# Optimization experiments

Measured on AMD Instinct MI355X. Metric: run time of the kernel, lower is better.

Reference implementation:

```python
import jax, jax.numpy as jnp
import numpy as np

NS, L, H = 8, 2048, 1024
M, E, K = 4096, 8, 2
EPS = 1e-9

def setup_inputs() -> dict:
    key = jax.random.key(0)
    ks = jax.random.split(key, 5)
    s = 0.02
    return {
        "x": jax.random.normal(ks[0], (NS, L, H), jnp.float32),
        "Wr": jax.random.normal(ks[1], (H, E), jnp.float32) * s,
        "br": jnp.zeros((E,), jnp.float32),
        "W1": jax.random.normal(ks[2], (E, H, M), jnp.float32) * s,
        "b1": jnp.zeros((E, M), jnp.float32),
        "W2": jax.random.normal(ks[3], (E, M, H), jnp.float32) * s,
        "b2": jnp.zeros((E, H), jnp.float32),
    }

def reference(x, Wr, br, W1, b1, W2, b2):
    ns, seq, h = x.shape
    flat = x.reshape(-1, h)                      # (N, H); grouping only reshapes, math is per-token
    logits = flat @ Wr + br                      # (N, E)
    probs = jax.nn.softmax(logits, axis=-1)
    vals, idx = jax.lax.top_k(probs, K)          # (N, K)
    w = vals / (jnp.sum(vals, axis=-1, keepdims=True) + EPS)
    out_acc = jnp.zeros_like(flat)
    weight_acc = jnp.zeros((flat.shape[0],), flat.dtype)
    for e in range(E):                           # fixed small expert loop
        we = jnp.sum(w * (idx == e), axis=-1)    # (N,) combine weight for expert e
        hmid = jax.nn.gelu(flat @ W1[e] + b1[e], approximate=False)
        y = hmid @ W2[e] + b2[e]
        out_acc = out_acc + we[:, None] * y
        weight_acc = weight_acc + we
    out = out_acc / (weight_acc[:, None] + EPS)
    return out.reshape(ns, seq, h)
```

## Files before the change

kernel.cpp:

```cpp
#include <hip/hip_runtime.h>
#include <hip/hip_bf16.h>
#include <math.h>

#define NTOK 16384
#define HDIM 1024
#define MDIM 4096
#define NEXP 8
#define EPSV 1e-9f
#define RTOK 32

typedef unsigned short u16;
typedef __attribute__((ext_vector_type(4))) float f32x4;
typedef __attribute__((ext_vector_type(8))) __bf16 bf16x8;
typedef __attribute__((ext_vector_type(8))) unsigned short u16x8;
typedef __attribute__((ext_vector_type(4))) unsigned short u16x4;

#define ASYNC_COPY16(gptr, lptr) \
    __builtin_amdgcn_global_load_lds( \
        (const __attribute__((address_space(1))) void*)(gptr), \
        (__attribute__((address_space(3))) void*)(lptr), 16, 0, 0)

static __device__ __forceinline__ u16 f2bf(float f) {
    unsigned int u = __builtin_bit_cast(unsigned int, f);
    u += 0x7fff + ((u >> 16) & 1);
    return (u16)(u >> 16);
}

static __device__ __forceinline__ float gelu_f(float v) {
    float z2 = -1.5957691216f * v * (1.f + 0.044715f * v * v);
    return v / (1.f + __expf(z2));
}

__global__ __launch_bounds__(256) void router_kernel(
    const float* __restrict__ x, const float* __restrict__ Wr,
    const float* __restrict__ br,
    int* __restrict__ counts, int* __restrict__ ltok, float* __restrict__ lcf,
    u16* __restrict__ xb)
{
    __shared__ int   lcount[NEXP];
    __shared__ int   lbase[NEXP];
    __shared__ int   ltokL[NEXP][RTOK];
    __shared__ float lcfL[NEXP][RTOK];

    int t = threadIdx.x;
    if (t < NEXP) lcount[t] = 0;
    __syncthreads();

    int wave = t >> 6, lane = t & 63;

    for (int it = 0; it < RTOK / 4; ++it) {
        int tok = blockIdx.x * RTOK + it * 4 + wave;
        const float* xr = x + (size_t)tok * HDIM + lane * 16;

        f32x4 xv[4];
        #pragma unroll
        for (int q = 0; q < 4; q++) xv[q] = *reinterpret_cast<const f32x4*>(xr + q * 4);

        u16x8 ob0, ob1;
        #pragma unroll
        for (int j = 0; j < 4; j++) {
            ob0[j]     = f2bf(xv[0][j]);
            ob0[4 + j] = f2bf(xv[1][j]);
            ob1[j]     = f2bf(xv[2][j]);
            ob1[4 + j] = f2bf(xv[3][j]);
        }
        u16* xo = xb + (size_t)tok * HDIM + lane * 16;
        *reinterpret_cast<u16x8*>(xo)     = ob0;
        *reinterpret_cast<u16x8*>(xo + 8) = ob1;

        f32x4 acc0 = {0.f, 0.f, 0.f, 0.f};
        f32x4 acc1 = {0.f, 0.f, 0.f, 0.f};
        #pragma unroll
        for (int q = 0; q < 4; q++) {
            #pragma unroll
            for (int j = 0; j < 4; j++) {
                int h = lane * 16 + q * 4 + j;
                const float* wrow = Wr + (size_t)h * NEXP;
                f32x4 w0 = *reinterpret_cast<const f32x4*>(wrow);
                f32x4 w1 = *reinterpret_cast<const f32x4*>(wrow + 4);
                acc0 += xv[q][j] * w0;
                acc1 += xv[q][j] * w1;
            }
        }
        float a[NEXP];
        #pragma unroll
        for (int e = 0; e < 4; e++) { a[e] = acc0[e]; a[4 + e] = acc1[e]; }
        #pragma unroll
        for (int e = 0; e < NEXP; e++) {
            #pragma unroll
            for (int s = 1; s < 64; s <<= 1) a[e] += __shfl_xor(a[e], s, 64);
        }
        if (lane == 0) {
            float l[NEXP], m = -1e30f;
            #pragma unroll
            for (int e = 0; e < NEXP; e++) { l[e] = a[e] + br[e]; m = fmaxf(m, l[e]); }
            float p[NEXP], s = 0.f;
            #pragma unroll
            for (int e = 0; e < NEXP; e++) { p[e] = expf(l[e] - m); s += p[e]; }
            int i0 = 0; float v0 = p[0];
            #pragma unroll
            for (int e = 1; e < NEXP; e++) if (p[e] > v0) { v0 = p[e]; i0 = e; }
            int i1 = -1; float v1 = -1.f;
            #pragma unroll
            for (int e = 0; e < NEXP; e++) if (e != i0 && p[e] > v1) { v1 = p[e]; i1 = e; }
            v0 /= s; v1 /= s;
            float sw = v0 + v1;
            float w0 = v0 / (sw + EPSV), w1 = v1 / (sw + EPSV);
            float wa = w0 + w1;
            float c0 = w0 / (wa + EPSV), c1 = w1 / (wa + EPSV);
            int q0 = atomicAdd(&lcount[i0], 1);
            ltokL[i0][q0] = tok; lcfL[i0][q0] = c0;
            int q1 = atomicAdd(&lcount[i1], 1);
            ltokL[i1][q1] = tok; lcfL[i1][q1] = c1;
        }
    }
    __syncthreads();
    if (t < NEXP) lbase[t] = atomicAdd(&counts[t], lcount[t]);
    __syncthreads();
    #pragma unroll
    for (int e = 0; e < NEXP; e++) {
        int n = lcount[e], b = lbase[e];
        for (int j = t; j < n; j += 256) {
            ltok[e * NTOK + b + j] = ltokL[e][j];
            lcf[e * NTOK + b + j]  = lcfL[e][j];
        }
    }
}

__global__ void bases_kernel(const int* __restrict__ counts, int* __restrict__ bases)
{
    if (threadIdx.x == 0) {
        int acc = 0;
        #pragma unroll
        for (int e = 0; e < NEXP; e++) { bases[e] = acc; acc += counts[e]; }
    }
}

__global__ __launch_bounds__(256) void transpose_cvt_kernel(
    const float* __restrict__ in, u16* __restrict__ out, int R, int C)
{
    __shared__ float tile[32][33];
    const float* ine = in + (size_t)blockIdx.z * R * C;
    u16* oute = out + (size_t)blockIdx.z * R * C;
    int r0 = blockIdx.y * 32, c0 = blockIdx.x * 32;
    int t = threadIdx.x;
    int r = t >> 3, cq = t & 7;
    f32x4 v = *reinterpret_cast<const f32x4*>(ine + (size_t)(r0 + r) * C + c0 + cq * 4);
    #pragma unroll
    for (int j = 0; j < 4; j++) tile[r][cq * 4 + j] = v[j];
    __syncthreads();
    int c = t >> 3, rq = t & 7;
    u16x4 o;
    #pragma unroll
    for (int j = 0; j < 4; j++) o[j] = f2bf(tile[rq * 4 + j][c]);
    *reinterpret_cast<u16x4*>(oute + (size_t)(c0 + c) * R + r0 + rq * 4) = o;
}

template<int EPI, int GX, int GY>
__global__ __launch_bounds__(256) void gemm_kernel(
    const u16* __restrict__ A,
    const u16* __restrict__ BT_all,
    const float* __restrict__ bias_all,
    const int* __restrict__ counts,
    const int* __restrict__ bases,
    const int* __restrict__ ltok,
    const float* __restrict__ lcf,
    u16* __restrict__ hmid,
    float* __restrict__ out,
    int K, int P, int Astride, int eStart)
{
    int gz = gridDim.z;
    int nwg = GX * GY * gz;
    int orig = blockIdx.x + GX * (blockIdx.y + GY * blockIdx.z);
    int q = nwg >> 3, r = nwg & 7;
    int xcd = orig & 7, sub = orig >> 3;
    int wgid = (xcd < r ? xcd * (q + 1) : r * (q + 1) + (xcd - r) * q) + sub;
    int bx = wgid & (GX - 1);
    int rem = wgid / GX;
    int by = rem & (GY - 1);
    int bz = rem / GY;

    int e = eStart + bz;
    int nrows = counts[e];
    int row0 = by * 128;
    if (row0 >= nrows) return;
    int p0 = bx * 128;
    int slotbase = bases[e];
    const u16*   BT   = BT_all + (size_t)e * P * K;
    const float* bias = bias_all + (size_t)e * P;
    const int*   lte  = ltok + (size_t)e * NTOK;
    const float* lcfe = lcf  + (size_t)e * NTOK;

    __shared__ u16 As[2][128][64];
    __shared__ u16 Bs[2][128][64];

    int t = threadIdx.x;
    int wv = t >> 6, lane = t & 63;
    int lrow8 = lane >> 3;
    int lcol8 = lane & 7;
    int schunk = lcol8 ^ lrow8;

    const u16* aptr[4];
    const u16* bptr[4];
    #pragma unroll
    for (int i = 0; i < 4; i++) {
        int pos  = row0 + wv * 32 + i * 8 + lrow8;
        int posc = min(pos, nrows - 1);
        int arow = (EPI == 0) ? lte[posc] : (slotbase + posc);
        aptr[i] = A + (size_t)arow * Astride + schunk * 8;
        int prow = p0 + wv * 32 + i * 8 + lrow8;
        bptr[i] = BT + (size_t)prow * K + schunk * 8;
    }

    int wr = (wv >> 1) * 64, wc = (wv & 1) * 64;
    int lr = lane & 15, lg = lane >> 4;
    int lr7 = lr & 7;

    f32x4 acc[4][4];
    #pragma unroll
    for (int m = 0; m < 4; m++)
        #pragma unroll
        for (int nn = 0; nn < 4; nn++) acc[m][nn] = (f32x4){0.f, 0.f, 0.f, 0.f};

    auto stage = [&](int buf, int k0) {
        #pragma unroll
        for (int i = 0; i < 4; i++) {
            ASYNC_COPY16(aptr[i] + k0, &As[buf][wv * 32 + i * 8][0]);
            ASYNC_COPY16(bptr[i] + k0, &Bs[buf][wv * 32 + i * 8][0]);
        }
    };

    stage(0, 0);
    __syncthreads();
    int nk = K >> 6;
    int cur = 0;
    for (int ks = 0; ks < nk; ks++) {
        if (ks + 1 < nk) stage(cur ^ 1, (ks + 1) << 6);
        #pragma unroll
        for (int kk = 0; kk < 64; kk += 32) {
            bf16x8 af[4], bfr[4];
            #pragma unroll
            for (int m = 0; m < 4; m++)
                af[m] = *reinterpret_cast<const bf16x8*>(
                    &As[cur][wr + m * 16 + lr][((((kk >> 3) + lg) ^ lr7)) * 8]);
            #pragma unroll
            for (int nn = 0; nn < 4; nn++)
                bfr[nn] = *reinterpret_cast<const bf16x8*>(
                    &Bs[cur][wc + nn * 16 + lr][((((kk >> 3) + lg) ^ lr7)) * 8]);
            #pragma unroll
            for (int m = 0; m < 4; m++)
                #pragma unroll
                for (int nn = 0; nn < 4; nn++)
                    acc[m][nn] = __builtin_amdgcn_mfma_f32_16x16x32_bf16(
                        af[m], bfr[nn], acc[m][nn], 0, 0, 0);
        }
        __syncthreads();
        cur ^= 1;
    }

    if (EPI == 0) {
        #pragma unroll
        for (int m = 0; m < 4; m++) {
            #pragma unroll
            for (int r2 = 0; r2 < 4; r2++) {
                int pos = row0 + wr + m * 16 + lg * 4 + r2;
                if (pos < nrows) {
                    size_t ho = (size_t)(slotbase + pos) * MDIM;
                    #pragma unroll
                    for (int nn = 0; nn < 4; nn++) {
                        int col = p0 + wc + nn * 16 + lr;
                        float v = acc[m][nn][r2] + bias[col];
                        hmid[ho + col] = f2bf(gelu_f(v));
                    }
                }
            }
        }
    } else {
        #pragma unroll
        for (int m = 0; m < 4; m++) {
            #pragma unroll
            for (int r2 = 0; r2 < 4; r2++) {
                int pos = row0 + wr + m * 16 + lg * 4 + r2;
                if (pos < nrows) {
                    int tokr = lte[pos];
                    float cf = lcfe[pos];
                    float* orow = out + (size_t)tokr * HDIM;
                    #pragma unroll
                    for (int nn = 0; nn < 4; nn++) {
                        int col = p0 + wc + nn * 16 + lr;
                        float v = (acc[m][nn][r2] + bias[col]) * cf;
                        atomicAdd(orow + col, v);
                    }
                }
            }
        }
    }
}

extern "C" void kernel_launch(void* const* d_in, const int* in_sizes, int n_in,
                              void* d_out, int out_size, void* d_ws, size_t ws_size,
                              hipStream_t stream)
{
    const float* x  = (const float*)d_in[0];
    const float* Wr = (const float*)d_in[1];
    const float* br = (const float*)d_in[2];
    const float* W1 = (const float*)d_in[3];
    const float* b1 = (const float*)d_in[4];
    const float* W2 = (const float*)d_in[5];
    const float* b2 = (const float*)d_in[6];
    float* out = (float*)d_out;

    char* ws = (char*)d_ws;
    size_t off = 0;
    auto alloc = [&](size_t bytes) {
        void* p = ws + off;
        off = (off + bytes + 255) & ~(size_t)255;
        return p;
    };
    int*   counts = (int*)  alloc(NEXP * 4);
    int*   bases  = (int*)  alloc(NEXP * 4);
    int*   ltok   = (int*)  alloc((size_t)NEXP * NTOK * 4);
    float* lcf    = (float*)alloc((size_t)NEXP * NTOK * 4);
    u16*   xb     = (u16*)  alloc((size_t)NTOK * HDIM * 2);
    u16*   w1t    = (u16*)  alloc((size_t)NEXP * MDIM * HDIM * 2);
    u16*   w2t    = (u16*)  alloc((size_t)NEXP * HDIM * MDIM * 2);
    size_t fixed_end = off;
    bool grouped = (ws_size >= fixed_end + (size_t)2 * NTOK * MDIM * 2);
    u16* hmid = (u16*)alloc((grouped ? (size_t)2 * NTOK : (size_t)NTOK) * MDIM * 2);

    hipMemsetAsync(counts, 0, NEXP * 4, stream);
    hipMemsetAsync(d_out, 0, (size_t)out_size * sizeof(float), stream);

    transpose_cvt_kernel<<<dim3(MDIM / 32, HDIM / 32, NEXP), 256, 0, stream>>>(W1, w1t, HDIM, MDIM);
    transpose_cvt_kernel<<<dim3(HDIM / 32, MDIM / 32, NEXP), 256, 0, stream>>>(W2, w2t, MDIM, HDIM);
    router_kernel<<<NTOK / RTOK, 256, 0, stream>>>(x, Wr, br, counts, ltok, lcf, xb);

    if (grouped) {
        bases_kernel<<<1, 64, 0, stream>>>(counts, bases);
        gemm_kernel<0, MDIM / 128, NTOK / 128>
            <<<dim3(MDIM / 128, NTOK / 128, NEXP), 256, 0, stream>>>(
            xb, w1t, b1, counts, bases, ltok, lcf, hmid, nullptr,
            HDIM, MDIM, HDIM, 0);
        gemm_kernel<1, HDIM / 128, NTOK / 128>
            <<<dim3(HDIM / 128, NTOK / 128, NEXP), 256, 0, stream>>>(
            hmid, w2t, b2, counts, bases, ltok, lcf, nullptr, out,
            MDIM, HDIM, MDIM, 0);
    } else {
        hipMemsetAsync(bases, 0, NEXP * 4, stream);
        for (int e = 0; e < NEXP; e++) {
            gemm_kernel<0, MDIM / 128, NTOK / 128>
                <<<dim3(MDIM / 128, NTOK / 128, 1), 256, 0, stream>>>(
                xb, w1t, b1, counts, bases, ltok, lcf, hmid, nullptr,
                HDIM, MDIM, HDIM, e);
            gemm_kernel<1, HDIM / 128, NTOK / 128>
                <<<dim3(HDIM / 128, NTOK / 128, 1), 256, 0, stream>>>(
                hmid, w2t, b2, counts, bases, ltok, lcf, nullptr, out,
                MDIM, HDIM, MDIM, e);
        }
    }
}
```

Before: 1.185 ms.

## Enlarge grouped GEMM tiles to 256x256 with 8 waves and explicit LDS/MFMA pipeline

```diff
diff --git a/kernel.cpp b/kernel.cpp
--- a/kernel.cpp
+++ b/kernel.cpp
@@ -156,8 +156,44 @@
     *reinterpret_cast<u16x4*>(oute + (size_t)(c0 + c) * R + r0 + rq * 4) = o;
 }
 
+#define SBAR() do { __builtin_amdgcn_sched_barrier(0); \
+                    __builtin_amdgcn_s_barrier(); \
+                    __builtin_amdgcn_sched_barrier(0); } while (0)
+
+#define CHUNK(ks) ((((ks) * 4 + lg) ^ lr7) * 8)
+
+#define READ_A(mlo) do { \
+    _Pragma("unroll") for (int i = 0; i < 4; i++) { \
+        afr[0][i] = *reinterpret_cast<const bf16x8*>(&As[buf][wm][(mlo + i) * 16 + lr][CHUNK(0)]); \
+        afr[1][i] = *reinterpret_cast<const bf16x8*>(&As[buf][wm][(mlo + i) * 16 + lr][CHUNK(1)]); \
+    } } while (0)
+
+#define READ_B(nlo) do { \
+    _Pragma("unroll") for (int j = 0; j < 2; j++) { \
+        bfr[0][j] = *reinterpret_cast<const bf16x8*>(&Bs[buf][wbh][wbr + (nlo + j) * 16 + lr][CHUNK(0)]); \
+        bfr[1][j] = *reinterpret_cast<const bf16x8*>(&Bs[buf][wbh][wbr + (nlo + j) * 16 + lr][CHUNK(1)]); \
+    } } while (0)
+
+#define MFMA_Q(mlo, nlo) do { \
+    __builtin_amdgcn_s_setprio(1); \
+    _Pragma("unroll") for (int ks = 0; ks < 2; ks++) \
+    _Pragma("unroll") for (int i = 0; i < 4; i++) \
+    _Pragma("unroll") for (int j = 0; j < 2; j++) \
+        acc[mlo + i][nlo + j] = __builtin_amdgcn_mfma_f32_16x16x32_bf16( \
+            afr[ks][i], bfr[ks][j], acc[mlo + i][nlo + j], 0, 0, 0); \
+    __builtin_amdgcn_s_setprio(0); \
+} while (0)
+
+#define STAGE_A(tau) do { int _b = (tau) & 1; size_t _k = (size_t)(tau) * 64; \
+    _Pragma("unroll") for (int i = 0; i < 4; i++) \
+        ASYNC_COPY16(aS[i] + _k, &As[_b][i >> 1][(i & 1) * 64 + wid * 8][0]); } while (0)
+
+#define STAGE_B(tau) do { int _b = (tau) & 1; size_t _k = (size_t)(tau) * 64; \
+    _Pragma("unroll") for (int i = 0; i < 4; i++) \
+        ASYNC_COPY16(bS[i] + _k, &Bs[_b][i >> 1][(i & 1) * 64 + wid * 8][0]); } while (0)
+
 template<int EPI, int GX, int GY>
-__global__ __launch_bounds__(256) void gemm_kernel(
+__global__ __launch_bounds__(512, 2) void gemm_kernel(
     const u16* __restrict__ A,
     const u16* __restrict__ BT_all,
     const float* __restrict__ bias_all,
@@ -172,9 +208,9 @@
     int gz = gridDim.z;
     int nwg = GX * GY * gz;
     int orig = blockIdx.x + GX * (blockIdx.y + GY * blockIdx.z);
-    int q = nwg >> 3, r = nwg & 7;
+    int qq = nwg >> 3, rr = nwg & 7;
     int xcd = orig & 7, sub = orig >> 3;
-    int wgid = (xcd < r ? xcd * (q + 1) : r * (q + 1) + (xcd - r) * q) + sub;
+    int wgid = (xcd < rr ? xcd * (qq + 1) : rr * (qq + 1) + (xcd - rr) * qq) + sub;
     int bx = wgid & (GX - 1);
     int rem = wgid / GX;
     int by = rem & (GY - 1);
@@ -182,93 +218,100 @@
 
     int e = eStart + bz;
     int nrows = counts[e];
-    int row0 = by * 128;
+    int row0 = by * 256;
     if (row0 >= nrows) return;
-    int p0 = bx * 128;
+    int p0 = bx * 256;
     int slotbase = bases[e];
     const u16*   BT   = BT_all + (size_t)e * P * K;
     const float* bias = bias_all + (size_t)e * P;
     const int*   lte  = ltok + (size_t)e * NTOK;
     const float* lcfe = lcf  + (size_t)e * NTOK;
 
-    __shared__ u16 As[2][128][64];
-    __shared__ u16 Bs[2][128][64];
+    __shared__ u16 As[2][2][128][64];
+    __shared__ u16 Bs[2][2][128][64];
 
     int t = threadIdx.x;
-    int wv = t >> 6, lane = t & 63;
-    int lrow8 = lane >> 3;
-    int lcol8 = lane & 7;
-    int schunk = lcol8 ^ lrow8;
-
-    const u16* aptr[4];
-    const u16* bptr[4];
+    int wid = t >> 6, lane = t & 63;
+    int wm = wid >> 2;
+    int wn = wid & 3;
+    int wbh = wn >> 1;
+    int wbr = (wn & 1) * 64;
+    int lr = lane & 15, lg = lane >> 4;
+    int lr7 = lr & 7;
+
+    int rl = t >> 3, ch = t & 7;
+    int sc = ch ^ (rl & 7);
+    const u16* aS[4];
+    const u16* bS[4];
     #pragma unroll
     for (int i = 0; i < 4; i++) {
-        int pos  = row0 + wv * 32 + i * 8 + lrow8;
+        int trow = (i >> 1) * 128 + (i & 1) * 64 + rl;
+        int pos  = row0 + trow;
         int posc = min(pos, nrows - 1);
         int arow = (EPI == 0) ? lte[posc] : (slotbase + posc);
-        aptr[i] = A + (size_t)arow * Astride + schunk * 8;
-        int prow = p0 + wv * 32 + i * 8 + lrow8;
-        bptr[i] = BT + (size_t)prow * K + schunk * 8;
-    }
-
-    int wr = (wv >> 1) * 64, wc = (wv & 1) * 64;
-    int lr = lane & 15, lg = lane >> 4;
-    int lr7 = lr & 7;
-
-    f32x4 acc[4][4];
+        aS[i] = A + (size_t)arow * Astride + sc * 8;
+        int prow = p0 + trow;
+        bS[i] = BT + (size_t)prow * K + sc * 8;
+    }
+
+    f32x4 acc[8][4];
     #pragma unroll
-    for (int m = 0; m < 4; m++)
+    for (int m = 0; m < 8; m++)
         #pragma unroll
         for (int nn = 0; nn < 4; nn++) acc[m][nn] = (f32x4){0.f, 0.f, 0.f, 0.f};
 
-    auto stage = [&](int buf, int k0) {
-        #pragma unroll
-        for (int i = 0; i < 4; i++) {
-            ASYNC_COPY16(aptr[i] + k0, &As[buf][wv * 32 + i * 8][0]);
-            ASYNC_COPY16(bptr[i] + k0, &Bs[buf][wv * 32 + i * 8][0]);
-        }
-    };
-
-    stage(0, 0);
-    __syncthreads();
     int nk = K >> 6;
-    int cur = 0;
-    for (int ks = 0; ks < nk; ks++) {
-        if (ks + 1 < nk) stage(cur ^ 1, (ks + 1) << 6);
-        #pragma unroll
-        for (int kk = 0; kk < 64; kk += 32) {
-            bf16x8 af[4], bfr[4];
-            #pragma unroll
-            for (int m = 0; m < 4; m++)
-                af[m] = *reinterpret_cast<const bf16x8*>(
-                    &As[cur][wr + m * 16 + lr][((((kk >> 3) + lg) ^ lr7)) * 8]);
-            #pragma unroll
-            for (int nn = 0; nn < 4; nn++)
-                bfr[nn] = *reinterpret_cast<const bf16x8*>(
-                    &Bs[cur][wc + nn * 16 + lr][((((kk >> 3) + lg) ^ lr7)) * 8]);
-            #pragma unroll
-            for (int m = 0; m < 4; m++)
-                #pragma unroll
-                for (int nn = 0; nn < 4; nn++)
-                    acc[m][nn] = __builtin_amdgcn_mfma_f32_16x16x32_bf16(
-                        af[m], bfr[nn], acc[m][nn], 0, 0, 0);
-        }
-        __syncthreads();
-        cur ^= 1;
+
+    STAGE_A(0);
+    STAGE_B(0);
+    if (nk > 1) { STAGE_A(1); }
+    __builtin_amdgcn_sched_barrier(0);
+    if (nk > 1) asm volatile("s_waitcnt vmcnt(4)" ::: "memory");
+    else        asm volatile("s_waitcnt vmcnt(0)" ::: "memory");
+    SBAR();
+
+    for (int tau = 0; tau < nk; ++tau) {
+        int buf = tau & 1;
+        bf16x8 afr[2][4], bfr[2][2];
+
+        READ_A(0);
+        READ_B(0);
+        if (tau + 1 < nk) { STAGE_B(tau + 1); }
+        SBAR();
+        MFMA_Q(0, 0);
+        SBAR();
+
+        READ_B(2);
+        SBAR();
+        MFMA_Q(0, 2);
+        SBAR();
+
+        READ_A(4);
+        SBAR();
+        MFMA_Q(4, 2);
+        SBAR();
+
+        READ_B(0);
+        if (tau + 2 < nk) { STAGE_A(tau + 2); }
+        SBAR();
+        MFMA_Q(4, 0);
+        __builtin_amdgcn_sched_barrier(0);
+        if (tau + 2 < nk) asm volatile("s_waitcnt vmcnt(4)" ::: "memory");
+        else              asm volatile("s_waitcnt vmcnt(0)" ::: "memory");
+        SBAR();
     }
 
     if (EPI == 0) {
         #pragma unroll
-        for (int m = 0; m < 4; m++) {
+        for (int m = 0; m < 8; m++) {
             #pragma unroll
             for (int r2 = 0; r2 < 4; r2++) {
-                int pos = row0 + wr + m * 16 + lg * 4 + r2;
+                int pos = row0 + wm * 128 + m * 16 + lg * 4 + r2;
                 if (pos < nrows) {
                     size_t ho = (size_t)(slotbase + pos) * MDIM;
                     #pragma unroll
                     for (int nn = 0; nn < 4; nn++) {
-                        int col = p0 + wc + nn * 16 + lr;
+                        int col = p0 + wn * 64 + nn * 16 + lr;
                         float v = acc[m][nn][r2] + bias[col];
                         hmid[ho + col] = f2bf(gelu_f(v));
                     }
@@ -277,17 +320,17 @@
         }
     } else {
         #pragma unroll
-        for (int m = 0; m < 4; m++) {
+        for (int m = 0; m < 8; m++) {
             #pragma unroll
             for (int r2 = 0; r2 < 4; r2++) {
-                int pos = row0 + wr + m * 16 + lg * 4 + r2;
+                int pos = row0 + wm * 128 + m * 16 + lg * 4 + r2;
                 if (pos < nrows) {
                     int tokr = lte[pos];
                     float cf = lcfe[pos];
                     float* orow = out + (size_t)tokr * HDIM;
                     #pragma unroll
                     for (int nn = 0; nn < 4; nn++) {
-                        int col = p0 + wc + nn * 16 + lr;
+                        int col = p0 + wn * 64 + nn * 16 + lr;
                         float v = (acc[m][nn][r2] + bias[col]) * cf;
                         atomicAdd(orow + col, v);
                     }
@@ -337,23 +380,23 @@
 
     if (grouped) {
         bases_kernel<<<1, 64, 0, stream>>>(counts, bases);
-        gemm_kernel<0, MDIM / 128, NTOK / 128>
-            <<<dim3(MDIM / 128, NTOK / 128, NEXP), 256, 0, stream>>>(
+        gemm_kernel<0, MDIM / 256, NTOK / 256>
+            <<<dim3(MDIM / 256, NTOK / 256, NEXP), 512, 0, stream>>>(
             xb, w1t, b1, counts, bases, ltok, lcf, hmid, nullptr,
             HDIM, MDIM, HDIM, 0);
-        gemm_kernel<1, HDIM / 128, NTOK / 128>
-            <<<dim3(HDIM / 128, NTOK / 128, NEXP), 256, 0, stream>>>(
+        gemm_kernel<1, HDIM / 256, NTOK / 256>
+            <<<dim3(HDIM / 256, NTOK / 256, NEXP), 512, 0, stream>>>(
             hmid, w2t, b2, counts, bases, ltok, lcf, nullptr, out,
             MDIM, HDIM, MDIM, 0);
     } else {
         hipMemsetAsync(bases, 0, NEXP * 4, stream);
         for (int e = 0; e < NEXP; e++) {
-            gemm_kernel<0, MDIM / 128, NTOK / 128>
-                <<<dim3(MDIM / 128, NTOK / 128, 1), 256, 0, stream>>>(
+            gemm_kernel<0, MDIM / 256, NTOK / 256>
+                <<<dim3(MDIM / 256, NTOK / 256, 1), 512, 0, stream>>>(
                 xb, w1t, b1, counts, bases, ltok, lcf, hmid, nullptr,
                 HDIM, MDIM, HDIM, e);
-            gemm_kernel<1, HDIM / 128, NTOK / 128>
-                <<<dim3(HDIM / 128, NTOK / 128, 1), 256, 0, stream>>>(
+            gemm_kernel<1, HDIM / 256, NTOK / 256>
+                <<<dim3(HDIM / 256, NTOK / 256, 1), 512, 0, stream>>>(
                 hmid, w2t, b2, counts, bases, ltok, lcf, nullptr, out,
                 MDIM, HDIM, MDIM, e);
         }
```

Result: faster. 1.122 ms (-5.3%).
